# Kernel tuning notes

Measured on AMD Instinct MI355X. Metric: run time of the kernel, lower is better.

## Reference

```python
import jax, jax.numpy as jnp
import numpy as np
import math

N = 16384
IN_F = 256
OUT_F = 64
EPS = 1e-6


def setup_inputs() -> dict:
    key = jax.random.key(0)
    k1, k2, k3, k4 = jax.random.split(key, 4)
    stdv = 1.0 / math.sqrt(OUT_F)
    inp = jax.random.normal(k1, (N, IN_F), dtype=jnp.float32)
    adj = jax.random.uniform(k2, (N, N), dtype=jnp.float32)
    weight = jax.random.uniform(k3, (IN_F, OUT_F), dtype=jnp.float32, minval=-stdv, maxval=stdv)
    bias = jax.random.uniform(k4, (OUT_F,), dtype=jnp.float32, minval=-stdv, maxval=stdv)
    return {"input": inp, "adj": adj, "weight": weight, "bias": bias, "p": 2}


def reference(input, adj, weight, bias, p):
    # support: [N, OUT_F]
    support = input @ weight
    mu = jnp.min(support)  # global scalar min
    pre_sup = support - mu + EPS  # >= EPS, safe for pow
    pre_top = pre_sup ** (p + 1)
    pre_down = pre_sup ** p
    # p-power mean aggregation: two adj matmuls sharing adj reads
    output = (adj @ pre_top) / (adj @ pre_down) + mu
    return output + bias
```

## Files before the change

### kernel.cpp

```cpp
#include <hip/hip_runtime.h>
#include <hip/hip_bf16.h>

typedef __attribute__((ext_vector_type(8))) short short8;
typedef __attribute__((ext_vector_type(4))) float f32x4;
typedef unsigned short u16;
typedef unsigned int u32;

#define NROWS 16384
#define KDIM 16384
#define EPS 1e-6f

__device__ __forceinline__ u16 f2bf(float x) {
    union { float f; u32 u; } v; v.f = x;
    u32 u = v.u;
    u32 r = (u + 0x7FFFu + ((u >> 16) & 1u)) >> 16;
    return (u16)r;
}

__device__ __forceinline__ void glds16(const void* g, void* l) {
    __builtin_amdgcn_global_load_lds(
        (const __attribute__((address_space(1))) void*)g,
        (__attribute__((address_space(3))) void*)l, 16, 0, 0);
}

__device__ __forceinline__ short cvbf(float x) {
    __hip_bfloat16 h = __float2bfloat16(x);
    return *(short*)&h;
}

__global__ __launch_bounds__(256) void wt_kernel(const float* __restrict__ W,
                                                 float* __restrict__ Wt) {
    int idx = blockIdx.x * 256 + threadIdx.x;
    int k = idx >> 6, c = idx & 63;
    Wt[c * 256 + k] = W[idx];
}

__global__ __launch_bounds__(256) void support_kernel(
    const float* __restrict__ inp, const float* __restrict__ Wt,
    float* __restrict__ sup)
{
    int tid = threadIdx.x;
    int col = tid & 63;
    int rr = tid >> 6;
    int rowbase = blockIdx.x * 32 + rr * 8;
    const float4* wt4 = (const float4*)(Wt + (size_t)col * 256);
    float acc[8];
#pragma unroll
    for (int i = 0; i < 8; ++i) acc[i] = 0.f;
    for (int k4 = 0; k4 < 64; ++k4) {
        float4 wv = wt4[k4];
#pragma unroll
        for (int i = 0; i < 8; ++i) {
            float4 iv = *((const float4*)(inp + (size_t)(rowbase + i) * 256) + k4);
            acc[i] += iv.x * wv.x + iv.y * wv.y + iv.z * wv.z + iv.w * wv.w;
        }
    }
#pragma unroll
    for (int i = 0; i < 8; ++i)
        sup[(size_t)(rowbase + i) * 64 + col] = acc[i];
}

__global__ __launch_bounds__(256) void min_part_kernel(
    const float* __restrict__ sup, float* __restrict__ partmin)
{
    __shared__ float wmin[4];
    int tid = threadIdx.x;
    const float4* s4 = (const float4*)sup;
    size_t idx = (size_t)blockIdx.x * 256 + tid;
    float m = 3.4e38f;
#pragma unroll
    for (int j = 0; j < 4; ++j) {
        float4 v = s4[idx + (size_t)j * 65536];
        m = fminf(m, fminf(fminf(v.x, v.y), fminf(v.z, v.w)));
    }
#pragma unroll
    for (int off = 32; off; off >>= 1) m = fminf(m, __shfl_down(m, off, 64));
    if ((tid & 63) == 0) wmin[tid >> 6] = m;
    __syncthreads();
    if (tid == 0)
        partmin[blockIdx.x] = fminf(fminf(wmin[0], wmin[1]), fminf(wmin[2], wmin[3]));
}

__global__ __launch_bounds__(256) void min_final_kernel(
    const float* __restrict__ partmin, float* __restrict__ mu)
{
    __shared__ float wmin[4];
    int tid = threadIdx.x;
    float m = partmin[tid];
#pragma unroll
    for (int off = 32; off; off >>= 1) m = fminf(m, __shfl_down(m, off, 64));
    if ((tid & 63) == 0) wmin[tid >> 6] = m;
    __syncthreads();
    if (tid == 0)
        mu[0] = fminf(fminf(wmin[0], wmin[1]), fminf(wmin[2], wmin[3]));
}

__global__ __launch_bounds__(256) void build_bt_kernel(
    const float* __restrict__ sup, const float* __restrict__ muptr,
    const int* __restrict__ pptr, u16* __restrict__ Bt)
{
    int k = blockIdx.x * 256 + threadIdx.x;
    float mu = *muptr;
    int p = *pptr;
    const float4* srow = (const float4*)(sup + (size_t)k * 64);
#pragma unroll
    for (int j = 0; j < 16; ++j) {
        float4 v = srow[j];
        float ss[4] = {v.x, v.y, v.z, v.w};
#pragma unroll
        for (int q = 0; q < 4; ++q) {
            int c = j * 4 + q;
            float s = ss[q] - mu + EPS;
            float d = 1.f;
            for (int i = 0; i < p; ++i) d *= s;
            Bt[(size_t)c * KDIM + k] = f2bf(d * s);
            Bt[(size_t)(c + 64) * KDIM + k] = f2bf(d);
        }
    }
}

#define BM 64
#define BN 128
#define BK 64
#define KH 8192
#define NTI 128

__global__ __launch_bounds__(512, 4) void gemm_kernel(
    const float* __restrict__ adj, const u16* __restrict__ Bt,
    float* __restrict__ Pp)
{
    __shared__ __align__(16) u16 Ash[2][BM * BK];
    __shared__ __align__(16) u16 Bsh[2][BN * BK];

    const int tid = threadIdx.x;
    const int rb = blockIdx.x >> 1;
    const int h  = blockIdx.x & 1;
    const size_t rowbase = (size_t)rb * BM;
    const size_t kbase   = (size_t)h * KH;

    const int ar = tid >> 3, ac = tid & 7;
    const float* asrc = adj + (rowbase + ar) * KDIM + kbase + ac * 8;
    const int awslot = ar * 8 + (ac ^ (ar & 7));

    const int ga0 = tid, ga1 = tid + 512;
    const int bn0 = ga0 >> 3, bx0 = (ga0 & 7) ^ (bn0 & 7);
    const int bn1 = ga1 >> 3, bx1 = (ga1 & 7) ^ (bn1 & 7);
    const u16* bsrc0 = Bt + (size_t)bn0 * KDIM + kbase + bx0 * 8;
    const u16* bsrc1 = Bt + (size_t)bn1 * KDIM + kbase + bx1 * 8;

    const int lane = tid & 63;
    const int w    = tid >> 6;
    const int wm   = w >> 2;
    const int wn   = w & 3;
    const int l15  = lane & 15, lg = lane >> 4;
    const int arow0 = wm * 32 + l15;
    const int arow1 = arow0 + 16;
    const int asw   = arow0 & 7;
    const int n0    = wn * 16 + l15;
    const int nd    = n0 + 64;
    const int bsw   = n0 & 7;

    f32x4 acc00 = {0.f, 0.f, 0.f, 0.f};
    f32x4 acc01 = acc00, acc10 = acc00, acc11 = acc00;

    auto gldsB = [&](int kt, int buf) {
        char* bb = (char*)Bsh[buf];
        const int koff = kt * BK;
        glds16(bsrc0 + koff, bb + ga0 * 16);
        glds16(bsrc1 + koff, bb + ga1 * 16);
    };
    auto loadA = [&](int kt, float4& x, float4& y) {
        const float4* p = (const float4*)(asrc + kt * BK);
        x = p[0]; y = p[1];
    };
    auto writeA = [&](const float4& x, const float4& y, int buf) {
        uint4 v;
        v.x = (u32)(u16)cvbf(x.x) | ((u32)(u16)cvbf(x.y) << 16);
        v.y = (u32)(u16)cvbf(x.z) | ((u32)(u16)cvbf(x.w) << 16);
        v.z = (u32)(u16)cvbf(y.x) | ((u32)(u16)cvbf(y.y) << 16);
        v.w = (u32)(u16)cvbf(y.z) | ((u32)(u16)cvbf(y.w) << 16);
        ((uint4*)Ash[buf])[awslot] = v;
    };
    auto compute = [&](int buf) {
        const short8* As8 = (const short8*)Ash[buf];
        const short8* Bs8 = (const short8*)Bsh[buf];
#pragma unroll
        for (int ks = 0; ks < 2; ++ks) {
            const int g = ks * 4 + lg;
            short8 a0 = As8[arow0 * 8 + (g ^ asw)];
            short8 a1 = As8[arow1 * 8 + (g ^ asw)];
            short8 bt_ = Bs8[n0 * 8 + (g ^ bsw)];
            short8 bd_ = Bs8[nd * 8 + (g ^ bsw)];
            acc00 = __builtin_amdgcn_mfma_f32_16x16x32_bf16(a0, bt_, acc00, 0, 0, 0);
            acc01 = __builtin_amdgcn_mfma_f32_16x16x32_bf16(a0, bd_, acc01, 0, 0, 0);
            acc10 = __builtin_amdgcn_mfma_f32_16x16x32_bf16(a1, bt_, acc10, 0, 0, 0);
            acc11 = __builtin_amdgcn_mfma_f32_16x16x32_bf16(a1, bd_, acc11, 0, 0, 0);
        }
    };

    float4 pa0, pa1;
    float4 pb0, pb1;

    loadA(0, pa0, pa1);
    gldsB(0, 0);
    writeA(pa0, pa1, 0);
    loadA(1, pa0, pa1);
    __syncthreads();

    for (int tt = 0; tt < NTI; tt += 2) {
        if (tt + 1 < NTI) gldsB(tt + 1, 1);
        if (tt + 2 < NTI) loadA(tt + 2, pb0, pb1);
        compute(0);
        if (tt + 1 < NTI) writeA(pa0, pa1, 1);
        __syncthreads();
        if (tt + 2 < NTI) gldsB(tt + 2, 0);
        if (tt + 3 < NTI) loadA(tt + 3, pa0, pa1);
        compute(1);
        if (tt + 2 < NTI) writeA(pb0, pb1, 0);
        __syncthreads();
    }

    float* pb = Pp + (size_t)blockIdx.x * (BM * BN);
#pragma unroll
    for (int q = 0; q < 4; ++q) {
        int r0 = wm * 32 + lg * 4 + q;
        int r1 = r0 + 16;
        pb[r0 * BN + n0] = acc00[q];
        pb[r0 * BN + nd] = acc01[q];
        pb[r1 * BN + n0] = acc10[q];
        pb[r1 * BN + nd] = acc11[q];
    }
}

__global__ __launch_bounds__(256) void reduce_kernel(
    const float* __restrict__ Pp, const float* __restrict__ bias,
    const float* __restrict__ muptr, float* __restrict__ out)
{
    int idx = blockIdx.x * 256 + threadIdx.x;
    int r = idx >> 6, c = idx & 63;
    int rb = r >> 6, rr = r & 63;
    const float* p0 = Pp + (size_t)(rb * 2) * (BM * BN) + rr * BN + c;
    const float* p1 = p0 + BM * BN;
    float T = p0[0]  + p1[0];
    float D = p0[64] + p1[64];
    out[idx] = T / D + muptr[0] + bias[c];
}

extern "C" void kernel_launch(void* const* d_in, const int* in_sizes, int n_in,
                              void* d_out, int out_size, void* d_ws, size_t ws_size,
                              hipStream_t stream)
{
    const float* inp  = (const float*)d_in[0];
    const float* adj  = (const float*)d_in[1];
    const float* W    = (const float*)d_in[2];
    const float* bias = (const float*)d_in[3];
    const int*   p    = (const int*)d_in[4];
    float* out = (float*)d_out;

    char* ws = (char*)d_ws;
    u16*   Bt      = (u16*)ws;
    float* partmin = (float*)(ws + (size_t)4 * 1024 * 1024);
    float* mu      = partmin + 256;
    float* Wt      = (float*)(ws + (size_t)4 * 1024 * 1024 + 4096);
    float* Pp      = (float*)(ws + (size_t)8 * 1024 * 1024);

    float* sup = out;

    wt_kernel       <<<64,   256, 0, stream>>>(W, Wt);
    support_kernel  <<<512,  256, 0, stream>>>(inp, Wt, sup);
    min_part_kernel <<<256,  256, 0, stream>>>(sup, partmin);
    min_final_kernel<<<1,    256, 0, stream>>>(partmin, mu);
    build_bt_kernel <<<64,   256, 0, stream>>>(sup, mu, p, Bt);
    gemm_kernel     <<<512,  512, 0, stream>>>(adj, Bt, Pp);
    reduce_kernel   <<<4096, 256, 0, stream>>>(Pp, bias, mu, out);
}
```

Before: 291.0 us.

## Triple-buffer GEMM LDS tiles with explicit waitcnt and one barrier per tile

Moves the adj-by-Bt GEMM main loop from double to triple LDS buffering, unrolled six tiles at a time with rotating register staging. Prefetch now runs two tiles ahead, and explicit s_waitcnt vmcnt/lgkmcnt plus a raw s_barrier replace __syncthreads, so each tile needs one barrier instead of a full drain. The aim is to hide global-load latency on the streamed fp32 adjacency. The cost is 50% more LDS per block, which may lower occupancy, and the hand-tuned wait counts must match the issued load counts exactly.

```diff
diff --git a/kernel.cpp b/kernel.cpp
--- a/kernel.cpp
+++ b/kernel.cpp
@@ -129,8 +129,8 @@
     const float* __restrict__ adj, const u16* __restrict__ Bt,
     float* __restrict__ Pp)
 {
-    __shared__ __align__(16) u16 Ash[2][BM * BK];
-    __shared__ __align__(16) u16 Bsh[2][BN * BK];
+    __shared__ __align__(16) u16 Ash[3][BM * BK];
+    __shared__ __align__(16) u16 Bsh[3][BN * BK];
 
     const int tid = threadIdx.x;
     const int rb = blockIdx.x >> 1;
@@ -198,27 +198,45 @@
         }
     };
 
-    float4 pa0, pa1;
-    float4 pb0, pb1;
+    float4 pa0, pa1, pb0, pb1;
 
     loadA(0, pa0, pa1);
     gldsB(0, 0);
+    asm volatile("s_waitcnt vmcnt(2)" ::: "memory");
     writeA(pa0, pa1, 0);
     loadA(1, pa0, pa1);
-    __syncthreads();
-
-    for (int tt = 0; tt < NTI; tt += 2) {
-        if (tt + 1 < NTI) gldsB(tt + 1, 1);
-        if (tt + 2 < NTI) loadA(tt + 2, pb0, pb1);
-        compute(0);
-        if (tt + 1 < NTI) writeA(pa0, pa1, 1);
-        __syncthreads();
-        if (tt + 2 < NTI) gldsB(tt + 2, 0);
-        if (tt + 3 < NTI) loadA(tt + 3, pa0, pa1);
-        compute(1);
-        if (tt + 2 < NTI) writeA(pb0, pb1, 0);
-        __syncthreads();
-    }
+    gldsB(1, 1);
+    asm volatile("s_waitcnt vmcnt(4)" ::: "memory");
+    asm volatile("s_waitcnt lgkmcnt(0)" ::: "memory");
+    __builtin_amdgcn_s_barrier();
+
+#define BODY(T, CUR, NXT, PRE, W0, W1, L0, L1)                          \
+    {                                                                   \
+        gldsB((T) + 2, (PRE));                                          \
+        loadA((T) + 2, L0, L1);                                         \
+        asm volatile("s_waitcnt vmcnt(4)" ::: "memory");                \
+        writeA(W0, W1, (NXT));                                          \
+        compute((CUR));                                                 \
+        asm volatile("s_waitcnt lgkmcnt(0)" ::: "memory");              \
+        __builtin_amdgcn_s_barrier();                                   \
+    }
+
+    for (int tt = 0; tt < NTI - 2; tt += 6) {
+        BODY(tt + 0, 0, 1, 2, pa0, pa1, pb0, pb1);
+        BODY(tt + 1, 1, 2, 0, pb0, pb1, pa0, pa1);
+        BODY(tt + 2, 2, 0, 1, pa0, pa1, pb0, pb1);
+        BODY(tt + 3, 0, 1, 2, pb0, pb1, pa0, pa1);
+        BODY(tt + 4, 1, 2, 0, pa0, pa1, pb0, pb1);
+        BODY(tt + 5, 2, 0, 1, pb0, pb1, pa0, pa1);
+    }
+#undef BODY
+
+    asm volatile("s_waitcnt vmcnt(0)" ::: "memory");
+    writeA(pa0, pa1, 1);
+    compute(0);
+    asm volatile("s_waitcnt lgkmcnt(0)" ::: "memory");
+    __builtin_amdgcn_s_barrier();
+    compute(1);
 
     float* pb = Pp + (size_t)blockIdx.x * (BM * BN);
 #pragma unroll
```

Measured after the change: 314.5 us. 8.1% more time.
